# Kernel tuning notes

Hardware: AMD Instinct MI355X
Metric: run time of the kernel (lower is better)

## Reference

```python
import jax, jax.numpy as jnp
import numpy as np

B = 131072  # batch size; feature dims 256->64->16->4 are hardcoded in the module


def setup_inputs() -> dict:
    key = jax.random.key(0)
    ks = jax.random.split(key, 7)
    return {
        "x": jax.random.normal(ks[0], (B, 256), dtype=jnp.float32),
        "w1": jax.random.normal(ks[1], (256, 64), dtype=jnp.float32),
        "b1": jax.random.normal(ks[2], (1, 64), dtype=jnp.float32),
        "w2": jax.random.normal(ks[3], (64, 16), dtype=jnp.float32),
        "b2": jax.random.normal(ks[4], (1, 16), dtype=jnp.float32),
        "w3": jax.random.normal(ks[5], (16, 4), dtype=jnp.float32),
        "b3": jax.random.normal(ks[6], (1, 4), dtype=jnp.float32),
    }


def reference(x, w1, b1, w2, b2, w3, b3):
    h = jax.nn.relu(x @ w1 + b1)          # [B, 64]
    h = jnp.tanh(h @ w2 + b2)             # [B, 16]
    logits = h @ w3 + b3                  # [B, 4]
    # Faithful to original soft(): softmax over the ENTIRE flattened tensor
    # (normalizes across batch AND class dims), then reshape back.
    y = jax.nn.softmax(logits.reshape(-1)).reshape(logits.shape)
    return y
```

## Files before the change

### kernel.cpp

```cpp
#include <hip/hip_runtime.h>
#include <math.h>


#define NBLOCKS (131072 / 64)

__global__ __launch_bounds__(256, 4)
void mlp_kernel(const float* __restrict__ x, const float* __restrict__ w1,
                const float* __restrict__ b1, const float* __restrict__ w2,
                const float* __restrict__ b2, const float* __restrict__ w3,
                const float* __restrict__ b3, float* __restrict__ out,
                float* __restrict__ wsum)
{
    __shared__ float xs[64 * 129];
    __shared__ float ws2[64 * 16];
    __shared__ float ws3[16 * 4];
    __shared__ float bsum[4];

    const int tid  = threadIdx.x;
    const int lane = tid & 63;
    const int wid  = tid >> 6;
    const int c0   = __builtin_amdgcn_readfirstlane(wid * 16);
    const int row0 = blockIdx.x * 64;

    for (int i = tid; i < 64 * 16; i += 256) ws2[i] = w2[i];
    if (tid < 64) ws3[tid] = w3[tid];

    float acc[16];
#pragma unroll
    for (int j = 0; j < 16; ++j) acc[j] = 0.0f;

    for (int p = 0; p < 2; ++p) {
        __syncthreads();
#pragma unroll
        for (int i = 0; i < 8; ++i) {
            const int idx = i * 256 + tid;
            const int r = idx >> 5;
            const int f = idx & 31;
            const float4 v = *(const float4*)(x + (size_t)(row0 + r) * 256 + p * 128 + f * 4);
            float* d = &xs[r * 129 + f * 4];
            d[0] = v.x; d[1] = v.y; d[2] = v.z; d[3] = v.w;
        }
        __syncthreads();

        const float* w1p = w1 + (size_t)p * 128 * 64 + c0;
        const float* xrow = &xs[lane * 129];
#pragma unroll 4
        for (int k = 0; k < 128; ++k) {
            const float xv = xrow[k];
            const float* wr = w1p + (size_t)k * 64;
#pragma unroll
            for (int j = 0; j < 16; ++j)
                acc[j] = fmaf(xv, wr[j], acc[j]);
        }
    }
    __syncthreads();

    float* hs = xs;
#pragma unroll
    for (int j = 0; j < 16; ++j)
        hs[lane * 65 + c0 + j] = fmaxf(acc[j] + b1[c0 + j], 0.0f);
    __syncthreads();

    const int r2  = wid * 16 + (lane >> 2);
    const int q   = lane & 3;

    float z2[4];
#pragma unroll
    for (int t = 0; t < 4; ++t) z2[t] = b2[4 * t + q];
#pragma unroll 8
    for (int c = 0; c < 64; ++c) {
        const float hv = hs[r2 * 65 + c];
#pragma unroll
        for (int t = 0; t < 4; ++t)
            z2[t] = fmaf(hv, ws2[c * 16 + 4 * t + q], z2[t]);
    }

    float lg[4] = {0.0f, 0.0f, 0.0f, 0.0f};
#pragma unroll
    for (int t = 0; t < 4; ++t) {
        const float th = tanhf(z2[t]);
        const int j = 4 * t + q;
#pragma unroll
        for (int o = 0; o < 4; ++o)
            lg[o] = fmaf(th, ws3[j * 4 + o], lg[o]);
    }
#pragma unroll
    for (int o = 0; o < 4; ++o) {
        lg[o] += __shfl_xor(lg[o], 1);
        lg[o] += __shfl_xor(lg[o], 2);
        lg[o] = expf(lg[o] + b3[o]);
    }
    if (q == 0)
        *(float4*)&out[(size_t)(row0 + r2) * 4] =
            make_float4(lg[0], lg[1], lg[2], lg[3]);

    float s = (lg[0] + lg[1] + lg[2] + lg[3]) * 0.25f;
#pragma unroll
    for (int off = 1; off < 64; off <<= 1) s += __shfl_xor(s, off);
    if (lane == 0) bsum[wid] = s;
    __syncthreads();
    if (tid == 0) atomicAdd(wsum, bsum[0] + bsum[1] + bsum[2] + bsum[3]);
}

__global__ __launch_bounds__(256)
void norm_kernel(float4* __restrict__ out, const float* __restrict__ wsum, int n4)
{
    const int i = blockIdx.x * 256 + threadIdx.x;
    if (i < n4) {
        const float inv = 1.0f / *wsum;
        float4 v = out[i];
        v.x *= inv; v.y *= inv; v.z *= inv; v.w *= inv;
        out[i] = v;
    }
}

extern "C" void kernel_launch(void* const* d_in, const int* in_sizes, int n_in,
                              void* d_out, int out_size, void* d_ws, size_t ws_size,
                              hipStream_t stream) {
    (void)in_sizes; (void)n_in; (void)ws_size;
    const float* x  = (const float*)d_in[0];
    const float* w1 = (const float*)d_in[1];
    const float* b1 = (const float*)d_in[2];
    const float* w2 = (const float*)d_in[3];
    const float* b2 = (const float*)d_in[4];
    const float* w3 = (const float*)d_in[5];
    const float* b3 = (const float*)d_in[6];
    float* out  = (float*)d_out;
    float* wsum = (float*)d_ws;

    hipMemsetAsync(wsum, 0, sizeof(float), stream);
    mlp_kernel<<<NBLOCKS, 256, 0, stream>>>(x, w1, b1, w2, b2, w3, b3, out, wsum);
    const int n4 = out_size >> 2;
    norm_kernel<<<(n4 + 255) / 256, 256, 0, stream>>>((float4*)out, wsum, n4);
}
```

Measured before the change: 265.1 us.

## Compute first layer with split-bf16 MFMA and enlarge blocks to 256 rows

Result: faster. 218.0 us (-17.8%).

```diff
diff --git a/kernel.cpp b/kernel.cpp
--- a/kernel.cpp
+++ b/kernel.cpp
@@ -2,104 +2,172 @@
 #include <math.h>
 
 
-#define NBLOCKS (131072 / 64)
-
-__global__ __launch_bounds__(256, 4)
+typedef __attribute__((ext_vector_type(8))) short bf16x8;
+typedef __attribute__((ext_vector_type(4))) float f32x4;
+
+#define WK 520
+#define HS 68
+#define NBLOCKS 512
+
+__device__ __forceinline__ short f2bf(float v) {
+    unsigned u = __float_as_uint(v);
+    unsigned r = (u + 0x7FFFu + ((u >> 16) & 1u)) >> 16;
+    return (short)r;
+}
+__device__ __forceinline__ float bf2f(short s) {
+    return __uint_as_float(((unsigned)(unsigned short)s) << 16);
+}
+
+__global__ __launch_bounds__(512, 4)
 void mlp_kernel(const float* __restrict__ x, const float* __restrict__ w1,
                 const float* __restrict__ b1, const float* __restrict__ w2,
                 const float* __restrict__ b2, const float* __restrict__ w3,
                 const float* __restrict__ b3, float* __restrict__ out,
                 float* __restrict__ wsum)
 {
-    __shared__ float xs[64 * 129];
+    __shared__ __align__(16) char smem[256 * HS * 4];
     __shared__ float ws2[64 * 16];
-    __shared__ float ws3[16 * 4];
-    __shared__ float bsum[4];
+    __shared__ float ws3[64];
+    __shared__ float bs1[64];
+    __shared__ float bsum[8];
+    short* wlds = (short*)smem;
+    float* hs   = (float*)smem;
 
     const int tid  = threadIdx.x;
     const int lane = tid & 63;
     const int wid  = tid >> 6;
-    const int c0   = __builtin_amdgcn_readfirstlane(wid * 16);
-    const int row0 = blockIdx.x * 64;
-
-    for (int i = tid; i < 64 * 16; i += 256) ws2[i] = w2[i];
+    const int quad = lane >> 4;
+    const int m16  = lane & 15;
+
+    for (int i = tid; i < 1024; i += 512) ws2[i] = w2[i];
     if (tid < 64) ws3[tid] = w3[tid];
-
-    float acc[16];
-#pragma unroll
-    for (int j = 0; j < 16; ++j) acc[j] = 0.0f;
-
-    for (int p = 0; p < 2; ++p) {
-        __syncthreads();
-#pragma unroll
-        for (int i = 0; i < 8; ++i) {
-            const int idx = i * 256 + tid;
-            const int r = idx >> 5;
-            const int f = idx & 31;
-            const float4 v = *(const float4*)(x + (size_t)(row0 + r) * 256 + p * 128 + f * 4);
-            float* d = &xs[r * 129 + f * 4];
-            d[0] = v.x; d[1] = v.y; d[2] = v.z; d[3] = v.w;
-        }
-        __syncthreads();
-
-        const float* w1p = w1 + (size_t)p * 128 * 64 + c0;
-        const float* xrow = &xs[lane * 129];
+    if (tid >= 64 && tid < 128) bs1[tid - 64] = b1[tid - 64];
+    {
+        const int n  = tid & 63;
+        const int kb = (tid >> 6) * 4;
+        for (int kk = kb; kk < 256; kk += 32) {
+            const float v0 = w1[(size_t)(kk + 0) * 64 + n];
+            const float v1 = w1[(size_t)(kk + 1) * 64 + n];
+            const float v2 = w1[(size_t)(kk + 2) * 64 + n];
+            const float v3 = w1[(size_t)(kk + 3) * 64 + n];
+            short4 hi, lo;
+            hi.x = f2bf(v0); lo.x = f2bf(v0 - bf2f(hi.x));
+            hi.y = f2bf(v1); lo.y = f2bf(v1 - bf2f(hi.y));
+            hi.z = f2bf(v2); lo.z = f2bf(v2 - bf2f(hi.z));
+            hi.w = f2bf(v3); lo.w = f2bf(v3 - bf2f(hi.w));
+            *(short4*)&wlds[n * WK + kk]       = hi;
+            *(short4*)&wlds[n * WK + 256 + kk] = lo;
+        }
+    }
+    __syncthreads();
+
+    const int row0 = blockIdx.x * 256 + wid * 32;
+    f32x4 acc[2][4];
+#pragma unroll
+    for (int mt = 0; mt < 2; ++mt)
+#pragma unroll
+        for (int t = 0; t < 4; ++t) acc[mt][t] = (f32x4)0.0f;
+
+#pragma unroll 2
+    for (int s = 0; s < 8; ++s) {
+        bf16x8 bh[4], bl[4];
+#pragma unroll
+        for (int t = 0; t < 4; ++t) {
+            const short* bp = &wlds[(t * 16 + m16) * WK + s * 32 + quad * 8];
+            bh[t] = *(const bf16x8*)bp;
+            bl[t] = *(const bf16x8*)(bp + 256);
+        }
+#pragma unroll
+        for (int mt = 0; mt < 2; ++mt) {
+            const float* xp = x + (size_t)(row0 + mt * 16 + m16) * 256
+                                + s * 32 + quad * 8;
+            const float4 v0 = *(const float4*)xp;
+            const float4 v1 = *(const float4*)(xp + 4);
+            const float f[8] = {v0.x, v0.y, v0.z, v0.w, v1.x, v1.y, v1.z, v1.w};
+            bf16x8 ah, al;
+#pragma unroll
+            for (int j = 0; j < 8; ++j) {
+                const short h = f2bf(f[j]);
+                ah[j] = h;
+                al[j] = f2bf(f[j] - bf2f(h));
+            }
+#pragma unroll
+            for (int t = 0; t < 4; ++t)
+                acc[mt][t] = __builtin_amdgcn_mfma_f32_16x16x32_bf16(
+                    ah, bh[t], acc[mt][t], 0, 0, 0);
+#pragma unroll
+            for (int t = 0; t < 4; ++t)
+                acc[mt][t] = __builtin_amdgcn_mfma_f32_16x16x32_bf16(
+                    al, bh[t], acc[mt][t], 0, 0, 0);
+#pragma unroll
+            for (int t = 0; t < 4; ++t)
+                acc[mt][t] = __builtin_amdgcn_mfma_f32_16x16x32_bf16(
+                    ah, bl[t], acc[mt][t], 0, 0, 0);
+        }
+    }
+    __syncthreads();
+
+#pragma unroll
+    for (int mt = 0; mt < 2; ++mt)
+#pragma unroll
+        for (int t = 0; t < 4; ++t) {
+            const float bc = bs1[t * 16 + m16];
+#pragma unroll
+            for (int r = 0; r < 4; ++r) {
+                const int rr = wid * 32 + mt * 16 + quad * 4 + r;
+                hs[rr * HS + t * 16 + m16] = fmaxf(acc[mt][t][r] + bc, 0.0f);
+            }
+        }
+    __syncthreads();
+
+    const int r2 = tid >> 1;
+    const int jq = (tid & 1) * 8;
+    float z2[8];
+#pragma unroll
+    for (int jj = 0; jj < 8; ++jj) z2[jj] = b2[jq + jj];
 #pragma unroll 4
-        for (int k = 0; k < 128; ++k) {
-            const float xv = xrow[k];
-            const float* wr = w1p + (size_t)k * 64;
-#pragma unroll
-            for (int j = 0; j < 16; ++j)
-                acc[j] = fmaf(xv, wr[j], acc[j]);
-        }
-    }
-    __syncthreads();
-
-    float* hs = xs;
-#pragma unroll
-    for (int j = 0; j < 16; ++j)
-        hs[lane * 65 + c0 + j] = fmaxf(acc[j] + b1[c0 + j], 0.0f);
-    __syncthreads();
-
-    const int r2  = wid * 16 + (lane >> 2);
-    const int q   = lane & 3;
-
-    float z2[4];
-#pragma unroll
-    for (int t = 0; t < 4; ++t) z2[t] = b2[4 * t + q];
-#pragma unroll 8
-    for (int c = 0; c < 64; ++c) {
-        const float hv = hs[r2 * 65 + c];
-#pragma unroll
-        for (int t = 0; t < 4; ++t)
-            z2[t] = fmaf(hv, ws2[c * 16 + 4 * t + q], z2[t]);
-    }
-
-    float lg[4] = {0.0f, 0.0f, 0.0f, 0.0f};
-#pragma unroll
-    for (int t = 0; t < 4; ++t) {
-        const float th = tanhf(z2[t]);
-        const int j = 4 * t + q;
-#pragma unroll
-        for (int o = 0; o < 4; ++o)
-            lg[o] = fmaf(th, ws3[j * 4 + o], lg[o]);
-    }
-#pragma unroll
-    for (int o = 0; o < 4; ++o) {
-        lg[o] += __shfl_xor(lg[o], 1);
-        lg[o] += __shfl_xor(lg[o], 2);
-        lg[o] = expf(lg[o] + b3[o]);
-    }
-    if (q == 0)
-        *(float4*)&out[(size_t)(row0 + r2) * 4] =
-            make_float4(lg[0], lg[1], lg[2], lg[3]);
-
-    float s = (lg[0] + lg[1] + lg[2] + lg[3]) * 0.25f;
+    for (int c = 0; c < 64; c += 4) {
+        const float4 h4 = *(const float4*)&hs[r2 * HS + c];
+        const float hv[4] = {h4.x, h4.y, h4.z, h4.w};
+#pragma unroll
+        for (int i = 0; i < 4; ++i)
+#pragma unroll
+            for (int jj = 0; jj < 8; ++jj)
+                z2[jj] = fmaf(hv[i], ws2[(c + i) * 16 + jq + jj], z2[jj]);
+    }
+    float l0 = 0.f, l1 = 0.f, l2 = 0.f, l3 = 0.f;
+#pragma unroll
+    for (int jj = 0; jj < 8; ++jj) {
+        const float th = tanhf(z2[jj]);
+        const int j = jq + jj;
+        l0 = fmaf(th, ws3[j * 4 + 0], l0);
+        l1 = fmaf(th, ws3[j * 4 + 1], l1);
+        l2 = fmaf(th, ws3[j * 4 + 2], l2);
+        l3 = fmaf(th, ws3[j * 4 + 3], l3);
+    }
+    l0 += __shfl_xor(l0, 1); l1 += __shfl_xor(l1, 1);
+    l2 += __shfl_xor(l2, 1); l3 += __shfl_xor(l3, 1);
+
+    float s = 0.0f;
+    if ((tid & 1) == 0) {
+        const float e0 = expf(l0 + b3[0]);
+        const float e1 = expf(l1 + b3[1]);
+        const float e2 = expf(l2 + b3[2]);
+        const float e3 = expf(l3 + b3[3]);
+        *(float4*)&out[(size_t)(blockIdx.x * 256 + r2) * 4] =
+            make_float4(e0, e1, e2, e3);
+        s = e0 + e1 + e2 + e3;
+    }
 #pragma unroll
     for (int off = 1; off < 64; off <<= 1) s += __shfl_xor(s, off);
     if (lane == 0) bsum[wid] = s;
     __syncthreads();
-    if (tid == 0) atomicAdd(wsum, bsum[0] + bsum[1] + bsum[2] + bsum[3]);
+    if (tid == 0) {
+        float tot = 0.0f;
+#pragma unroll
+        for (int i = 0; i < 8; ++i) tot += bsum[i];
+        atomicAdd(wsum, tot);
+    }
 }
 
 __global__ __launch_bounds__(256)
@@ -129,7 +197,7 @@
     float* wsum = (float*)d_ws;
 
     hipMemsetAsync(wsum, 0, sizeof(float), stream);
-    mlp_kernel<<<NBLOCKS, 256, 0, stream>>>(x, w1, b1, w2, b2, w3, b3, out, wsum);
+    mlp_kernel<<<NBLOCKS, 512, 0, stream>>>(x, w1, b1, w2, b2, w3, b3, out, wsum);
     const int n4 = out_size >> 2;
     norm_kernel<<<(n4 + 255) / 256, 256, 0, stream>>>((float4*)out, wsum, n4);
 }
```
